# Performance work log

Measured on AMD Instinct MI355X. Metric: run time of the kernel, lower is better.

Reference implementation:

```python
import jax, jax.numpy as jnp
import numpy as np

L1_COST = 1000.0
ENTROPY_COST = 5e-05


def setup_inputs() -> dict:
    key = jax.random.key(0)
    k1, k2 = jax.random.split(key)
    inputs = jax.random.normal(k1, (8, 4096, 256), dtype=jnp.float32)
    # xavier_uniform for [K, D]: bound = sqrt(6/(K+D))
    K, D = 1024, 256
    bound = np.sqrt(6.0 / (K + D)).astype(np.float32)
    codebook = jax.random.uniform(k2, (K, D), dtype=jnp.float32, minval=-bound, maxval=bound)
    return {"inputs": inputs, "codebook": codebook}


def reference(inputs, codebook):
    D = codebook.shape[1]
    flat = inputs.reshape(-1, D)                                  # [N, D]
    norm_C = codebook / jnp.linalg.norm(codebook, axis=1, keepdims=True)   # [K, D]
    flat = flat / jnp.linalg.norm(flat, axis=1, keepdims=True)    # [N, D]
    distances = jax.nn.softmax(flat @ norm_C.T, axis=1)           # [N, K]
    reconstruction = (distances @ norm_C).reshape(inputs.shape)   # [B, S, D]
    # l1_loss(distances, zeros) == mean(|distances|)
    l1 = jnp.mean(jnp.abs(distances))
    # entropy term: mean_i sum_k [ -log_softmax(distances) @ distances.T ]_{ik}
    # = mean_i ( -log_softmax(distances)_i . colsum(distances) ), an O(N*K) equivalent
    log_sm = jax.nn.log_softmax(distances, axis=1)                # [N, K]
    col_sum = jnp.sum(distances, axis=0)                          # [K]
    entropy = jnp.mean(-(log_sm @ col_sum))
    loss = L1_COST * l1 + ENTROPY_COST * entropy
    return reconstruction, loss
```

## Files before the change

### kernel.cpp

```cpp
#include <hip/hip_runtime.h>
#include <cstdint>

#define N_ROWS 32768
#define KDIM 1024
#define DDIM 256

typedef __attribute__((ext_vector_type(8))) short bf16x8;
typedef __attribute__((ext_vector_type(4))) float f32x4;

__device__ __forceinline__ unsigned short f2bf(float f) {
  unsigned int u = __float_as_uint(f);
  u += 0x7FFFu + ((u >> 16) & 1u);
  return (unsigned short)(u >> 16);
}
__device__ __forceinline__ float bf2f(unsigned short b) {
  return __uint_as_float((unsigned int)b << 16);
}

__device__ __forceinline__ void gload_lds16(const void* g, void* l) {
  __builtin_amdgcn_global_load_lds(
      (const __attribute__((address_space(1))) unsigned int*)(uintptr_t)g,
      (__attribute__((address_space(3))) unsigned int*)(unsigned int)(uintptr_t)l,
      16, 0, 0);
}


__global__ __launch_bounds__(256) void k_norm_cb(const float* __restrict__ cb,
                                                 unsigned short* __restrict__ Cn,
                                                 unsigned short* __restrict__ CnT,
                                                 float* __restrict__ m_g) {
  __shared__ float msh[4][256];
  const int wid = threadIdx.x >> 6, lane = threadIdx.x & 63;
  const int k = blockIdx.x * 4 + wid;
  float4 v = ((const float4*)(cb + (size_t)k * DDIM))[lane];
  float s = v.x * v.x + v.y * v.y + v.z * v.z + v.w * v.w;
#pragma unroll
  for (int m = 32; m; m >>= 1) s += __shfl_xor(s, m, 64);
  const float rn = 1.0f / sqrtf(s);
  ushort4 p;
  p.x = f2bf(v.x * rn); p.y = f2bf(v.y * rn);
  p.z = f2bf(v.z * rn); p.w = f2bf(v.w * rn);
  const int kb = lane >> 3;
  const int physA = ((lane & 7) >> 1) ^ (k & 3);
  *(ushort4*)(Cn + (size_t)(k >> 6) * 16384 + kb * 2048 + (k & 63) * 32 + physA * 8 + (lane & 1) * 4) = p;
  const int sgl = k >> 5, c31 = k & 31, ch = c31 >> 3, cw = c31 & 7;
  const unsigned short pv[4] = {p.x, p.y, p.z, p.w};
#pragma unroll
  for (int j = 0; j < 4; ++j) {
    const int d = lane * 4 + j;
    CnT[(size_t)sgl * 8192 + d * 32 + ((ch ^ j) * 8) + cw] = pv[j];
    msh[wid][d] = bf2f(pv[j]);
  }
  __syncthreads();
  const int tid = threadIdx.x;
  if (tid < 256) atomicAdd(&m_g[tid], msh[0][tid] + msh[1][tid] + msh[2][tid] + msh[3][tid]);
}

__global__ __launch_bounds__(256) void k_gram(const unsigned short* __restrict__ CnT,
                                              unsigned short* __restrict__ Mn) {
  __shared__ unsigned short T[4][8192];
  const int tid = threadIdx.x, wv = tid >> 6, lane = tid & 63;
  const int l15 = lane & 15, l4 = lane >> 4;
  const int ab = blockIdx.x;
  const int xsw = l4 ^ (l15 & 3);
  f32x4 acc[4] = {};
#define STAGE_T(KS, SLOT)                                                            \
  do {                                                                               \
    _Pragma("unroll") for (int i_ = 0; i_ < 4; ++i_) {                               \
      const int o_ = i_ * 2048 + tid * 8;                                            \
      gload_lds16(CnT + (size_t)(KS) * 8192 + o_, (char*)T[SLOT] + (size_t)o_ * 2);  \
    }                                                                                \
  } while (0)
  STAGE_T(0, 0); STAGE_T(1, 1); STAGE_T(2, 2);
  for (int ks = 0; ks < 32; ++ks) {
    if (ks <= 29)      asm volatile("s_waitcnt vmcnt(8)" ::: "memory");
    else if (ks == 30) asm volatile("s_waitcnt vmcnt(4)" ::: "memory");
    else               asm volatile("s_waitcnt vmcnt(0)" ::: "memory");
    __builtin_amdgcn_s_barrier();
    __builtin_amdgcn_sched_barrier(0);
    const unsigned short* B = T[ks & 3];
    bf16x8 a = *(const bf16x8*)&B[(ab * 16 + l15) * 32 + xsw * 8];
#pragma unroll
    for (int ni = 0; ni < 4; ++ni) {
      const int d = wv * 64 + ni * 16 + l15;
      bf16x8 b = *(const bf16x8*)&B[d * 32 + xsw * 8];
      acc[ni] = __builtin_amdgcn_mfma_f32_16x16x32_bf16(a, b, acc[ni], 0, 0, 0);
    }
    __builtin_amdgcn_s_barrier();
    __builtin_amdgcn_sched_barrier(0);
    if (ks <= 28) STAGE_T(ks + 3, (ks + 3) & 3);
  }
#undef STAGE_T
#pragma unroll
  for (int ni = 0; ni < 4; ++ni)
#pragma unroll
    for (int reg = 0; reg < 4; ++reg) {
      const int a_ = ab * 16 + l4 * 4 + reg;
      const int b_ = wv * 64 + ni * 16 + l15;
      Mn[(size_t)(b_ >> 6) * 16384 + (a_ >> 5) * 2048 + (b_ & 63) * 32 +
         ((((a_ & 31) >> 3) ^ (b_ & 3)) * 8) + (a_ & 7)] = f2bf(acc[ni][reg]);
    }
}

__global__ __launch_bounds__(512, 2) void k_all(const float* __restrict__ x,
                                                const unsigned short* __restrict__ Cn,
                                                const unsigned short* __restrict__ CnT,
                                                const unsigned short* __restrict__ Mn,
                                                const float* __restrict__ m_g,
                                                float* __restrict__ colsum_g,
                                                float* __restrict__ accL,
                                                int* __restrict__ cnt2,
                                                float* __restrict__ out) {
  __shared__ unsigned short Cb[4][16384];
  __shared__ unsigned short Ps[128 * 72];
  __shared__ float csl[1024];
  __shared__ float u_sh[128], t_sh[128], irl[128];
  __shared__ float lse_sh[2];
  __shared__ float sh1[4], sh2[4];
  __shared__ int lastf;

  const int tid = threadIdx.x, wid = tid >> 6, lane = tid & 63;
  const int l15 = lane & 15, l4 = lane >> 4;
  const int wm = wid >> 1, wn = wid & 1;
  const int rb = blockIdx.x;
  if (tid < 128) t_sh[tid] = 0.f;
  for (int j = tid; j < 1024; j += 512) csl[j] = 0.f;

#define STAGE32(SRC, DST)                                          \
  do {                                                             \
    _Pragma("unroll") for (int i_ = 0; i_ < 4; ++i_) {             \
      const int off_ = i_ * 8192 + wid * 1024 + lane * 16;         \
      gload_lds16((const char*)(SRC) + off_, (char*)(DST) + off_); \
    }                                                              \
  } while (0)

  STAGE32(Mn, Cb[2]);
  STAGE32((const char*)Mn + 32768, Cb[3]);

  unsigned short* Xs = &Cb[0][0];
  const float4 mv = ((const float4*)m_g)[lane];
#pragma unroll
  for (int p16 = 0; p16 < 16; ++p16) {
    const int row = p16 * 8 + wid;
    float4 v = ((const float4*)(x + (size_t)(rb * 128 + row) * DDIM))[lane];
    float s = v.x * v.x + v.y * v.y + v.z * v.z + v.w * v.w;
#pragma unroll
    for (int m = 32; m; m >>= 1) s += __shfl_xor(s, m, 64);
    const float rn = 1.0f / sqrtf(s);
    ushort4 p;
    p.x = f2bf(v.x * rn); p.y = f2bf(v.y * rn);
    p.z = f2bf(v.z * rn); p.w = f2bf(v.w * rn);
    *(ushort4*)&Xs[(lane >> 3) * 4096 + row * 32 + (lane & 7) * 4] = p;
    float ud = bf2f(p.x) * mv.x + bf2f(p.y) * mv.y + bf2f(p.z) * mv.z + bf2f(p.w) * mv.w;
#pragma unroll
    for (int m = 32; m; m >>= 1) ud += __shfl_xor(ud, m, 64);
    if (lane == 0) u_sh[row] = ud;
  }
  __syncthreads();
  bf16x8 areg[2][8];
#pragma unroll
  for (int mi = 0; mi < 2; ++mi)
#pragma unroll
    for (int kb = 0; kb < 8; ++kb)
      areg[mi][kb] = *(const bf16x8*)&Xs[kb * 4096 + (wm * 32 + mi * 16 + l15) * 32 + l4 * 8];

  const int xsw = l4 ^ (l15 & 3);

  float tacc[2][4] = {{0.f, 0.f, 0.f, 0.f}, {0.f, 0.f, 0.f, 0.f}};
  auto t_step = [&](const unsigned short* Sm, int bbase) {
    f32x4 Y[2][2] = {};
#pragma unroll
    for (int kb = 0; kb < 8; ++kb) {
      bf16x8 b0 = *(const bf16x8*)&Sm[kb * 2048 + (wn * 32 + l15) * 32 + xsw * 8];
      bf16x8 b1 = *(const bf16x8*)&Sm[kb * 2048 + (wn * 32 + 16 + l15) * 32 + xsw * 8];
#pragma unroll
      for (int mi = 0; mi < 2; ++mi) {
        Y[mi][0] = __builtin_amdgcn_mfma_f32_16x16x32_bf16(areg[mi][kb], b0, Y[mi][0], 0, 0, 0);
        Y[mi][1] = __builtin_amdgcn_mfma_f32_16x16x32_bf16(areg[mi][kb], b1, Y[mi][1], 0, 0, 0);
      }
    }
#pragma unroll
    for (int mi = 0; mi < 2; ++mi)
#pragma unroll
      for (int ni = 0; ni < 2; ++ni) {
        const int b = bbase + wn * 32 + ni * 16 + l15;
#pragma unroll
        for (int reg = 0; reg < 4; ++reg) {
          const int row = wm * 32 + mi * 16 + l4 * 4 + reg;
          const float xv = bf2f(Xs[(b >> 5) * 4096 + row * 32 + (b & 31)]);
          tacc[mi][reg] += Y[mi][ni][reg] * xv;
        }
      }
  };
  t_step(Cb[2], 0);
  __builtin_amdgcn_s_barrier();
  __builtin_amdgcn_sched_barrier(0);
  STAGE32((const char*)Mn + 65536, Cb[2]);
  t_step(Cb[3], 64);
  asm volatile("s_waitcnt vmcnt(0)" ::: "memory");
  __builtin_amdgcn_s_barrier();
  __builtin_amdgcn_sched_barrier(0);
  STAGE32((const char*)Mn + 98304, Cb[3]);
  t_step(Cb[2], 128);
  asm volatile("s_waitcnt vmcnt(0)" ::: "memory");
  __builtin_amdgcn_s_barrier();
  __builtin_amdgcn_sched_barrier(0);
  STAGE32(Cn, Cb[2]);
  t_step(Cb[3], 192);
  __builtin_amdgcn_s_barrier();
  __builtin_amdgcn_sched_barrier(0);
  STAGE32(CnT, Cb[3]);

#pragma unroll
  for (int mi = 0; mi < 2; ++mi)
#pragma unroll
    for (int reg = 0; reg < 4; ++reg) {
#pragma unroll
      for (int m = 1; m < 16; m <<= 1) tacc[mi][reg] += __shfl_xor(tacc[mi][reg], m, 64);
    }
  if (l15 == 0) {
#pragma unroll
    for (int mi = 0; mi < 2; ++mi)
#pragma unroll
      for (int reg = 0; reg < 4; ++reg)
        atomicAdd(&t_sh[wm * 32 + mi * 16 + l4 * 4 + reg], tacc[mi][reg]);
  }
  asm volatile("s_waitcnt lgkmcnt(0)" ::: "memory");
  __builtin_amdgcn_s_barrier();
  if (tid < 128) {
    const float uu = u_sh[tid], tt = t_sh[tid];
    const float r = (float)KDIM + uu + 0.5f * tt;
    const float ir = 1.0f / r;
    irl[tid] = ir;
    const float q = (float)KDIM + 2.0f * uu + 2.0f * tt;
    float lse = logf((float)(KDIM + 1) + 0.5f * q * ir * ir);
#pragma unroll
    for (int m = 32; m; m >>= 1) lse += __shfl_xor(lse, m, 64);
    if ((tid & 63) == 0) lse_sh[tid >> 6] = lse;
  }
  asm volatile("s_waitcnt lgkmcnt(0)" ::: "memory");
  __builtin_amdgcn_s_barrier();
  f32x4 ir2[2];
#pragma unroll
  for (int mi = 0; mi < 2; ++mi)
    ir2[mi] = *(const f32x4*)&irl[wm * 32 + mi * 16 + l4 * 4];
  asm volatile("s_waitcnt vmcnt(4)" ::: "memory");
  __builtin_amdgcn_s_barrier();
  __builtin_amdgcn_sched_barrier(0);

  f32x4 O[2][8] = {};
  const int psw_r = l15 >> 1;
  for (int kt = 0; kt < 16; ++kt) {
    const int cslot = (kt & 1) ? 0 : 2;
    const int tslot = cslot | 1;
    const int nslot = (kt & 1) ? 2 : 0;
    if (kt < 15) {
      STAGE32((const char*)Cn + (size_t)(kt + 1) * 32768, Cb[nslot]);
      STAGE32((const char*)CnT + (size_t)(kt + 1) * 32768, Cb[nslot + 1]);
    }
    f32x4 S[2][2] = {};
#pragma unroll
    for (int kb = 0; kb < 8; ++kb) {
      bf16x8 b[2];
#pragma unroll
      for (int ni = 0; ni < 2; ++ni)
        b[ni] = *(const bf16x8*)&Cb[cslot][kb * 2048 + (wn * 32 + ni * 16 + l15) * 32 + xsw * 8];
#pragma unroll
      for (int mi = 0; mi < 2; ++mi)
#pragma unroll
        for (int ni = 0; ni < 2; ++ni)
          S[mi][ni] = __builtin_amdgcn_mfma_f32_16x16x32_bf16(areg[mi][kb], b[ni], S[mi][ni], 0, 0, 0);
    }
    float cs[2] = {0.f, 0.f};
#pragma unroll
    for (int mi = 0; mi < 2; ++mi)
#pragma unroll
      for (int reg = 0; reg < 4; ++reg) {
        const int row = wm * 32 + mi * 16 + l4 * 4 + reg;
        const int pswz = (l4 * 2 + (reg >> 1)) & 7;
#pragma unroll
        for (int ni = 0; ni < 2; ++ni) {
          const float e = __expf(S[mi][ni][reg]);
          const int chl = wn * 4 + ni * 2 + (l15 >> 3);
          Ps[row * 72 + ((chl ^ pswz) * 8) + (l15 & 7)] = f2bf(e);
          cs[ni] += e * ir2[mi][reg];
        }
      }
#pragma unroll
    for (int ni = 0; ni < 2; ++ni) {
      float v = cs[ni];
      v += __shfl_xor(v, 16, 64);
      v += __shfl_xor(v, 32, 64);
      if (lane < 16) atomicAdd(&csl[kt * 64 + wn * 32 + ni * 16 + l15], v);
    }
    if (kt < 15) asm volatile("s_waitcnt vmcnt(8) lgkmcnt(0)" ::: "memory");
    else         asm volatile("s_waitcnt vmcnt(0) lgkmcnt(0)" ::: "memory");
    __builtin_amdgcn_s_barrier();
    __builtin_amdgcn_sched_barrier(0);
#pragma unroll
    for (int kb2 = 0; kb2 < 2; ++kb2) {
      bf16x8 a2[2], b2[8];
#pragma unroll
      for (int mi = 0; mi < 2; ++mi) {
        const int row = wm * 32 + mi * 16 + l15;
        a2[mi] = *(const bf16x8*)&Ps[row * 72 + (((kb2 * 4 + l4) ^ psw_r) * 8)];
      }
#pragma unroll
      for (int ni = 0; ni < 8; ++ni) {
        const int d = wn * 128 + ni * 16 + l15;
        b2[ni] = *(const bf16x8*)&Cb[tslot][kb2 * 8192 + d * 32 + xsw * 8];
      }
#pragma unroll
      for (int mi = 0; mi < 2; ++mi)
#pragma unroll
        for (int ni = 0; ni < 8; ++ni)
          O[mi][ni] = __builtin_amdgcn_mfma_f32_16x16x32_bf16(a2[mi], b2[ni], O[mi][ni], 0, 0, 0);
    }
    if (kt < 15) asm volatile("s_waitcnt vmcnt(4)" ::: "memory");
    else         asm volatile("s_waitcnt vmcnt(0)" ::: "memory");
    __builtin_amdgcn_s_barrier();
    __builtin_amdgcn_sched_barrier(0);
  }

#pragma unroll
  for (int mi = 0; mi < 2; ++mi)
#pragma unroll
    for (int reg = 0; reg < 4; ++reg) {
      const int row = wm * 32 + mi * 16 + l4 * 4 + reg;
      const float irv = ir2[mi][reg];
#pragma unroll
      for (int ni = 0; ni < 8; ++ni) {
        const int d = wn * 128 + ni * 16 + l15;
        out[(size_t)(rb * 128 + row) * DDIM + d] = O[mi][ni][reg] * irv;
      }
    }
  for (int j = tid; j < 1024; j += 512) atomicAdd(&colsum_g[j], csl[j]);
  if (tid == 0) atomicAdd(accL, lse_sh[0] + lse_sh[1]);

  if (tid == 0) {
    __threadfence();
    const int old = __hip_atomic_fetch_add(cnt2, 1, __ATOMIC_ACQ_REL, __HIP_MEMORY_SCOPE_AGENT);
    lastf = (old == 255);
  }
  __syncthreads();
  if (lastf) {
    if (tid < 256) {
      float s = 0.f, q = 0.f;
#pragma unroll
      for (int j = 0; j < 4; ++j) {
        const float c = __hip_atomic_load(&colsum_g[tid + j * 256], __ATOMIC_RELAXED, __HIP_MEMORY_SCOPE_AGENT);
        s += c; q += c * c;
      }
#pragma unroll
      for (int m = 1; m < 64; m <<= 1) {
        s += __shfl_xor(s, m, 64);
        q += __shfl_xor(q, m, 64);
      }
      if (lane == 0) { sh1[tid >> 6] = s; sh2[tid >> 6] = q; }
    }
    __syncthreads();
    if (tid == 0) {
      const double S = (double)sh1[0] + sh1[1] + sh1[2] + sh1[3];
      const double Q = (double)sh2[0] + sh2[1] + sh2[2] + sh2[3];
      const double L = __hip_atomic_load(accL, __ATOMIC_RELAXED, __HIP_MEMORY_SCOPE_AGENT);
      const double entropy = (S * L - Q) / (double)N_ROWS;
      const double l1 = S / ((double)N_ROWS * (double)KDIM);
      out[(size_t)N_ROWS * DDIM] = (float)(1000.0 * l1 + 5e-5 * entropy);
    }
  }
#undef STAGE32
}

extern "C" void kernel_launch(void* const* d_in, const int* in_sizes, int n_in,
                              void* d_out, int out_size, void* d_ws, size_t ws_size,
                              hipStream_t stream) {
  const float* x = (const float*)d_in[0];
  const float* cb = (const float*)d_in[1];
  float* out = (float*)d_out;
  char* ws = (char*)d_ws;

  unsigned short* Cn  = (unsigned short*)(ws + 0);
  unsigned short* CnT = (unsigned short*)(ws + 524288);
  unsigned short* Mn  = (unsigned short*)(ws + 1048576);
  float* colsum_g     = (float*)(ws + 1179648);
  float* m_g          = (float*)(ws + 1183744);
  float* accL         = (float*)(ws + 1184768);
  int* cnt2           = (int*)(ws + 1184772);

  hipMemsetAsync(ws + 1179648, 0, 5128, stream);
  k_norm_cb<<<256, 256, 0, stream>>>(cb, Cn, CnT, m_g);
  k_gram<<<16, 256, 0, stream>>>(CnT, Mn);
  k_all<<<256, 512, 0, stream>>>(x, Cn, CnT, Mn, m_g, colsum_g, accL, cnt2, out);
}
```

Before: 182.9 us.

## Double waves per block in gram and fused kernels, splitting column tiles across waves

Both k_gram and k_all now launch 1024 threads (16 waves) instead of 256/512. Each wave computes a narrower slice of the output and score tiles, and the staging loops and wait counts are rescaled to match. The goal is more waves per CU so MFMA work and LDS and global loads can overlap better. In exchange each B fragment loaded from LDS feeds fewer MFMAs, and the tighter register budget under launch bounds of (1024, 4) risks spills.

```diff
diff --git a/kernel.cpp b/kernel.cpp
--- a/kernel.cpp
+++ b/kernel.cpp
@@ -56,61 +56,50 @@
   if (tid < 256) atomicAdd(&m_g[tid], msh[0][tid] + msh[1][tid] + msh[2][tid] + msh[3][tid]);
 }
 
-__global__ __launch_bounds__(256) void k_gram(const unsigned short* __restrict__ CnT,
-                                              unsigned short* __restrict__ Mn) {
+__global__ __launch_bounds__(1024) void k_gram(const unsigned short* __restrict__ CnT,
+                                               unsigned short* __restrict__ Mn) {
   __shared__ unsigned short T[4][8192];
   const int tid = threadIdx.x, wv = tid >> 6, lane = tid & 63;
   const int l15 = lane & 15, l4 = lane >> 4;
   const int ab = blockIdx.x;
   const int xsw = l4 ^ (l15 & 3);
-  f32x4 acc[4] = {};
-#define STAGE_T(KS, SLOT)                                                            \
-  do {                                                                               \
-    _Pragma("unroll") for (int i_ = 0; i_ < 4; ++i_) {                               \
-      const int o_ = i_ * 2048 + tid * 8;                                            \
-      gload_lds16(CnT + (size_t)(KS) * 8192 + o_, (char*)T[SLOT] + (size_t)o_ * 2);  \
-    }                                                                                \
-  } while (0)
+  f32x4 acc = {};
+#define STAGE_T(KS, SLOT) \
+  gload_lds16(CnT + (size_t)(KS) * 8192 + tid * 8, (char*)T[SLOT] + (size_t)tid * 16)
   STAGE_T(0, 0); STAGE_T(1, 1); STAGE_T(2, 2);
   for (int ks = 0; ks < 32; ++ks) {
-    if (ks <= 29)      asm volatile("s_waitcnt vmcnt(8)" ::: "memory");
-    else if (ks == 30) asm volatile("s_waitcnt vmcnt(4)" ::: "memory");
+    if (ks <= 29)      asm volatile("s_waitcnt vmcnt(2)" ::: "memory");
+    else if (ks == 30) asm volatile("s_waitcnt vmcnt(1)" ::: "memory");
     else               asm volatile("s_waitcnt vmcnt(0)" ::: "memory");
     __builtin_amdgcn_s_barrier();
     __builtin_amdgcn_sched_barrier(0);
     const unsigned short* B = T[ks & 3];
     bf16x8 a = *(const bf16x8*)&B[(ab * 16 + l15) * 32 + xsw * 8];
-#pragma unroll
-    for (int ni = 0; ni < 4; ++ni) {
-      const int d = wv * 64 + ni * 16 + l15;
-      bf16x8 b = *(const bf16x8*)&B[d * 32 + xsw * 8];
-      acc[ni] = __builtin_amdgcn_mfma_f32_16x16x32_bf16(a, b, acc[ni], 0, 0, 0);
-    }
+    bf16x8 b = *(const bf16x8*)&B[(wv * 16 + l15) * 32 + xsw * 8];
+    acc = __builtin_amdgcn_mfma_f32_16x16x32_bf16(a, b, acc, 0, 0, 0);
     __builtin_amdgcn_s_barrier();
     __builtin_amdgcn_sched_barrier(0);
     if (ks <= 28) STAGE_T(ks + 3, (ks + 3) & 3);
   }
 #undef STAGE_T
 #pragma unroll
-  for (int ni = 0; ni < 4; ++ni)
-#pragma unroll
-    for (int reg = 0; reg < 4; ++reg) {
-      const int a_ = ab * 16 + l4 * 4 + reg;
-      const int b_ = wv * 64 + ni * 16 + l15;
-      Mn[(size_t)(b_ >> 6) * 16384 + (a_ >> 5) * 2048 + (b_ & 63) * 32 +
-         ((((a_ & 31) >> 3) ^ (b_ & 3)) * 8) + (a_ & 7)] = f2bf(acc[ni][reg]);
-    }
-}
-
-__global__ __launch_bounds__(512, 2) void k_all(const float* __restrict__ x,
-                                                const unsigned short* __restrict__ Cn,
-                                                const unsigned short* __restrict__ CnT,
-                                                const unsigned short* __restrict__ Mn,
-                                                const float* __restrict__ m_g,
-                                                float* __restrict__ colsum_g,
-                                                float* __restrict__ accL,
-                                                int* __restrict__ cnt2,
-                                                float* __restrict__ out) {
+  for (int reg = 0; reg < 4; ++reg) {
+    const int a_ = ab * 16 + l4 * 4 + reg;
+    const int b_ = wv * 16 + l15;
+    Mn[(size_t)(b_ >> 6) * 16384 + (a_ >> 5) * 2048 + (b_ & 63) * 32 +
+       ((((a_ & 31) >> 3) ^ (b_ & 3)) * 8) + (a_ & 7)] = f2bf(acc[reg]);
+  }
+}
+
+__global__ __launch_bounds__(1024, 4) void k_all(const float* __restrict__ x,
+                                                 const unsigned short* __restrict__ Cn,
+                                                 const unsigned short* __restrict__ CnT,
+                                                 const unsigned short* __restrict__ Mn,
+                                                 const float* __restrict__ m_g,
+                                                 float* __restrict__ colsum_g,
+                                                 float* __restrict__ accL,
+                                                 int* __restrict__ cnt2,
+                                                 float* __restrict__ out) {
   __shared__ unsigned short Cb[4][16384];
   __shared__ unsigned short Ps[128 * 72];
   __shared__ float csl[1024];
@@ -121,15 +110,15 @@
 
   const int tid = threadIdx.x, wid = tid >> 6, lane = tid & 63;
   const int l15 = lane & 15, l4 = lane >> 4;
-  const int wm = wid >> 1, wn = wid & 1;
+  const int wm = wid >> 2, wn = wid & 3;
   const int rb = blockIdx.x;
   if (tid < 128) t_sh[tid] = 0.f;
-  for (int j = tid; j < 1024; j += 512) csl[j] = 0.f;
+  if (tid < 1024) csl[tid] = 0.f;
 
 #define STAGE32(SRC, DST)                                          \
   do {                                                             \
-    _Pragma("unroll") for (int i_ = 0; i_ < 4; ++i_) {             \
-      const int off_ = i_ * 8192 + wid * 1024 + lane * 16;         \
+    _Pragma("unroll") for (int i_ = 0; i_ < 2; ++i_) {             \
+      const int off_ = i_ * 16384 + tid * 16;                      \
       gload_lds16((const char*)(SRC) + off_, (char*)(DST) + off_); \
     }                                                              \
   } while (0)
@@ -140,8 +129,8 @@
   unsigned short* Xs = &Cb[0][0];
   const float4 mv = ((const float4*)m_g)[lane];
 #pragma unroll
-  for (int p16 = 0; p16 < 16; ++p16) {
-    const int row = p16 * 8 + wid;
+  for (int p8 = 0; p8 < 8; ++p8) {
+    const int row = p8 * 16 + wid;
     float4 v = ((const float4*)(x + (size_t)(rb * 128 + row) * DDIM))[lane];
     float s = v.x * v.x + v.y * v.y + v.z * v.z + v.w * v.w;
 #pragma unroll
@@ -168,28 +157,22 @@
 
   float tacc[2][4] = {{0.f, 0.f, 0.f, 0.f}, {0.f, 0.f, 0.f, 0.f}};
   auto t_step = [&](const unsigned short* Sm, int bbase) {
-    f32x4 Y[2][2] = {};
+    f32x4 Y[2] = {};
 #pragma unroll
     for (int kb = 0; kb < 8; ++kb) {
-      bf16x8 b0 = *(const bf16x8*)&Sm[kb * 2048 + (wn * 32 + l15) * 32 + xsw * 8];
-      bf16x8 b1 = *(const bf16x8*)&Sm[kb * 2048 + (wn * 32 + 16 + l15) * 32 + xsw * 8];
-#pragma unroll
-      for (int mi = 0; mi < 2; ++mi) {
-        Y[mi][0] = __builtin_amdgcn_mfma_f32_16x16x32_bf16(areg[mi][kb], b0, Y[mi][0], 0, 0, 0);
-        Y[mi][1] = __builtin_amdgcn_mfma_f32_16x16x32_bf16(areg[mi][kb], b1, Y[mi][1], 0, 0, 0);
-      }
-    }
+      bf16x8 b0 = *(const bf16x8*)&Sm[kb * 2048 + (wn * 16 + l15) * 32 + xsw * 8];
+#pragma unroll
+      for (int mi = 0; mi < 2; ++mi)
+        Y[mi] = __builtin_amdgcn_mfma_f32_16x16x32_bf16(areg[mi][kb], b0, Y[mi], 0, 0, 0);
+    }
+    const int b = bbase + wn * 16 + l15;
 #pragma unroll
     for (int mi = 0; mi < 2; ++mi)
 #pragma unroll
-      for (int ni = 0; ni < 2; ++ni) {
-        const int b = bbase + wn * 32 + ni * 16 + l15;
-#pragma unroll
-        for (int reg = 0; reg < 4; ++reg) {
-          const int row = wm * 32 + mi * 16 + l4 * 4 + reg;
-          const float xv = bf2f(Xs[(b >> 5) * 4096 + row * 32 + (b & 31)]);
-          tacc[mi][reg] += Y[mi][ni][reg] * xv;
-        }
+      for (int reg = 0; reg < 4; ++reg) {
+        const int row = wm * 32 + mi * 16 + l4 * 4 + reg;
+        const float xv = bf2f(Xs[(b >> 5) * 4096 + row * 32 + (b & 31)]);
+        tacc[mi][reg] += Y[mi][reg] * xv;
       }
   };
   t_step(Cb[2], 0);
@@ -244,11 +227,11 @@
 #pragma unroll
   for (int mi = 0; mi < 2; ++mi)
     ir2[mi] = *(const f32x4*)&irl[wm * 32 + mi * 16 + l4 * 4];
-  asm volatile("s_waitcnt vmcnt(4)" ::: "memory");
-  __builtin_amdgcn_s_barrier();
-  __builtin_amdgcn_sched_barrier(0);
-
-  f32x4 O[2][8] = {};
+  asm volatile("s_waitcnt vmcnt(2)" ::: "memory");
+  __builtin_amdgcn_s_barrier();
+  __builtin_amdgcn_sched_barrier(0);
+
+  f32x4 O[2][4] = {};
   const int psw_r = l15 >> 1;
   for (int kt = 0; kt < 16; ++kt) {
     const int cslot = (kt & 1) ? 0 : 2;
@@ -258,65 +241,53 @@
       STAGE32((const char*)Cn + (size_t)(kt + 1) * 32768, Cb[nslot]);
       STAGE32((const char*)CnT + (size_t)(kt + 1) * 32768, Cb[nslot + 1]);
     }
-    f32x4 S[2][2] = {};
+    f32x4 S[2] = {};
 #pragma unroll
     for (int kb = 0; kb < 8; ++kb) {
-      bf16x8 b[2];
-#pragma unroll
-      for (int ni = 0; ni < 2; ++ni)
-        b[ni] = *(const bf16x8*)&Cb[cslot][kb * 2048 + (wn * 32 + ni * 16 + l15) * 32 + xsw * 8];
+      bf16x8 b = *(const bf16x8*)&Cb[cslot][kb * 2048 + (wn * 16 + l15) * 32 + xsw * 8];
 #pragma unroll
       for (int mi = 0; mi < 2; ++mi)
-#pragma unroll
-        for (int ni = 0; ni < 2; ++ni)
-          S[mi][ni] = __builtin_amdgcn_mfma_f32_16x16x32_bf16(areg[mi][kb], b[ni], S[mi][ni], 0, 0, 0);
-    }
-    float cs[2] = {0.f, 0.f};
+        S[mi] = __builtin_amdgcn_mfma_f32_16x16x32_bf16(areg[mi][kb], b, S[mi], 0, 0, 0);
+    }
+    const int chl = wn * 2 + (l15 >> 3);
+    float cs = 0.f;
 #pragma unroll
     for (int mi = 0; mi < 2; ++mi)
 #pragma unroll
       for (int reg = 0; reg < 4; ++reg) {
         const int row = wm * 32 + mi * 16 + l4 * 4 + reg;
         const int pswz = (l4 * 2 + (reg >> 1)) & 7;
-#pragma unroll
-        for (int ni = 0; ni < 2; ++ni) {
-          const float e = __expf(S[mi][ni][reg]);
-          const int chl = wn * 4 + ni * 2 + (l15 >> 3);
-          Ps[row * 72 + ((chl ^ pswz) * 8) + (l15 & 7)] = f2bf(e);
-          cs[ni] += e * ir2[mi][reg];
-        }
-      }
-#pragma unroll
-    for (int ni = 0; ni < 2; ++ni) {
-      float v = cs[ni];
-      v += __shfl_xor(v, 16, 64);
-      v += __shfl_xor(v, 32, 64);
-      if (lane < 16) atomicAdd(&csl[kt * 64 + wn * 32 + ni * 16 + l15], v);
-    }
-    if (kt < 15) asm volatile("s_waitcnt vmcnt(8) lgkmcnt(0)" ::: "memory");
+        const float e = __expf(S[mi][reg]);
+        Ps[row * 72 + ((chl ^ pswz) * 8) + (l15 & 7)] = f2bf(e);
+        cs += e * ir2[mi][reg];
+      }
+    cs += __shfl_xor(cs, 16, 64);
+    cs += __shfl_xor(cs, 32, 64);
+    if (lane < 16) atomicAdd(&csl[kt * 64 + wn * 16 + l15], cs);
+    if (kt < 15) asm volatile("s_waitcnt vmcnt(4) lgkmcnt(0)" ::: "memory");
     else         asm volatile("s_waitcnt vmcnt(0) lgkmcnt(0)" ::: "memory");
     __builtin_amdgcn_s_barrier();
     __builtin_amdgcn_sched_barrier(0);
 #pragma unroll
     for (int kb2 = 0; kb2 < 2; ++kb2) {
-      bf16x8 a2[2], b2[8];
+      bf16x8 a2[2], b2[4];
 #pragma unroll
       for (int mi = 0; mi < 2; ++mi) {
         const int row = wm * 32 + mi * 16 + l15;
         a2[mi] = *(const bf16x8*)&Ps[row * 72 + (((kb2 * 4 + l4) ^ psw_r) * 8)];
       }
 #pragma unroll
-      for (int ni = 0; ni < 8; ++ni) {
-        const int d = wn * 128 + ni * 16 + l15;
+      for (int ni = 0; ni < 4; ++ni) {
+        const int d = wn * 64 + ni * 16 + l15;
         b2[ni] = *(const bf16x8*)&Cb[tslot][kb2 * 8192 + d * 32 + xsw * 8];
       }
 #pragma unroll
       for (int mi = 0; mi < 2; ++mi)
 #pragma unroll
-        for (int ni = 0; ni < 8; ++ni)
+        for (int ni = 0; ni < 4; ++ni)
           O[mi][ni] = __builtin_amdgcn_mfma_f32_16x16x32_bf16(a2[mi], b2[ni], O[mi][ni], 0, 0, 0);
     }
-    if (kt < 15) asm volatile("s_waitcnt vmcnt(4)" ::: "memory");
+    if (kt < 15) asm volatile("s_waitcnt vmcnt(2)" ::: "memory");
     else         asm volatile("s_waitcnt vmcnt(0)" ::: "memory");
     __builtin_amdgcn_s_barrier();
     __builtin_amdgcn_sched_barrier(0);
@@ -329,12 +300,12 @@
       const int row = wm * 32 + mi * 16 + l4 * 4 + reg;
       const float irv = ir2[mi][reg];
 #pragma unroll
-      for (int ni = 0; ni < 8; ++ni) {
-        const int d = wn * 128 + ni * 16 + l15;
+      for (int ni = 0; ni < 4; ++ni) {
+        const int d = wn * 64 + ni * 16 + l15;
         out[(size_t)(rb * 128 + row) * DDIM + d] = O[mi][ni][reg] * irv;
       }
     }
-  for (int j = tid; j < 1024; j += 512) atomicAdd(&colsum_g[j], csl[j]);
+  if (tid < 1024) atomicAdd(&colsum_g[tid], csl[tid]);
   if (tid == 0) atomicAdd(accL, lse_sh[0] + lse_sh[1]);
 
   if (tid == 0) {
@@ -389,6 +360,6 @@
 
   hipMemsetAsync(ws + 1179648, 0, 5128, stream);
   k_norm_cb<<<256, 256, 0, stream>>>(cb, Cn, CnT, m_g);
-  k_gram<<<16, 256, 0, stream>>>(CnT, Mn);
-  k_all<<<256, 512, 0, stream>>>(x, Cn, CnT, Mn, m_g, colsum_g, accL, cnt2, out);
-}
+  k_gram<<<16, 1024, 0, stream>>>(CnT, Mn);
+  k_all<<<256, 1024, 0, stream>>>(x, Cn, CnT, Mn, m_g, colsum_g, accL, cnt2, out);
+}
```

New measurement: 207.6 us. 13.5% more time.
